# Optimization experiments

Measured on AMD Instinct MI355X. Metric: run time of the kernel, lower is better.

## Reference

```python
import jax, jax.numpy as jnp
import numpy as np

N_NODES = 100000
N_EDGES = 1600000
D_IN = 128
D_HID = 128
N_CLASSES = 4
N_GRAPHS = 512


def setup_inputs() -> dict:
    key = jax.random.key(0)
    ks = jax.random.split(key, 10)
    x = jax.random.normal(ks[0], (N_NODES, D_IN), dtype=jnp.float32)
    edge_index = jax.random.randint(ks[1], (2, N_EDGES), 0, N_NODES, dtype=jnp.int64)
    batch = jnp.sort(jax.random.randint(ks[2], (N_NODES,), 0, N_GRAPHS, dtype=jnp.int64))
    s = 1.0 / np.sqrt(D_IN)
    W1l = jax.random.uniform(ks[3], (D_HID, D_IN), jnp.float32, -s, s)
    W1r = jax.random.uniform(ks[4], (D_HID, D_IN), jnp.float32, -s, s)
    b1 = jnp.zeros((D_HID,), jnp.float32)
    s2 = 1.0 / np.sqrt(D_HID)
    W2l = jax.random.uniform(ks[5], (D_HID, D_HID), jnp.float32, -s2, s2)
    W2r = jax.random.uniform(ks[6], (D_HID, D_HID), jnp.float32, -s2, s2)
    b2 = jnp.zeros((D_HID,), jnp.float32)
    Wlin = jax.random.uniform(ks[7], (N_CLASSES, D_HID), jnp.float32, -s2, s2)
    blin = jax.random.uniform(ks[8], (N_CLASSES,), jnp.float32, -s2, s2)
    return {"x": x, "edge_index": edge_index, "batch": batch,
            "W1l": W1l, "b1": b1, "W1r": W1r,
            "W2l": W2l, "b2": b2, "W2r": W2r,
            "Wlin": Wlin, "blin": blin}


def _sage_conv(x, src, dst, deg_inv, W_l, b, W_r):
    # mean-aggregate neighbor features (messages flow src -> dst)
    agg = jax.ops.segment_sum(x[src], dst, num_segments=N_NODES) * deg_inv
    return agg @ W_l.T + b + x @ W_r.T


def reference(x, edge_index, batch, W1l, b1, W1r, W2l, b2, W2r, Wlin, blin):
    src, dst = edge_index[0], edge_index[1]
    ones = jnp.ones((src.shape[0],), x.dtype)
    deg = jax.ops.segment_sum(ones, dst, num_segments=N_NODES)
    deg_inv = (1.0 / jnp.maximum(deg, 1.0))[:, None]

    h = jax.nn.relu(_sage_conv(x, src, dst, deg_inv, W1l, b1, W1r))
    h = jax.nn.relu(_sage_conv(h, src, dst, deg_inv, W2l, b2, W2r))

    # global mean pool over graphs
    gsum = jax.ops.segment_sum(h, batch, num_segments=N_GRAPHS)
    gcnt = jax.ops.segment_sum(jnp.ones((N_NODES,), h.dtype), batch, num_segments=N_GRAPHS)
    pooled = gsum / jnp.maximum(gcnt, 1.0)[:, None]

    # dropout is identity in eval mode
    return pooled @ Wlin.T + blin
```

## Files before the change

kernel.cpp:

```cpp
#include <hip/hip_runtime.h>
#include <hip/hip_bf16.h>


#define NN 100000
#define NE 1600000
#define DH 128
#define NG 512
#define CSTRIDE 48
#define NBKT 8
#define BKT_SZ 12500
#define NSLICE 256
#define ESLICE 6250

#define PSUM_SCALE  1048576.0f
#define PSUM_INV    (1.0f/1048576.0f)

typedef __hip_bfloat16 bf16;
typedef __bf16 bf16x8 __attribute__((ext_vector_type(8)));
typedef float  f32x4  __attribute__((ext_vector_type(4)));
typedef float  f32x2  __attribute__((ext_vector_type(2)));
typedef unsigned char u8;

__device__ __forceinline__ void bf8_to_f(uint4 q, float* w) {
    union { unsigned u; float f; } t;
    t.u = q.x << 16;          w[0] = t.f;
    t.u = q.x & 0xffff0000u;  w[1] = t.f;
    t.u = q.y << 16;          w[2] = t.f;
    t.u = q.y & 0xffff0000u;  w[3] = t.f;
    t.u = q.z << 16;          w[4] = t.f;
    t.u = q.z & 0xffff0000u;  w[5] = t.f;
    t.u = q.w << 16;          w[6] = t.f;
    t.u = q.w & 0xffff0000u;  w[7] = t.f;
}

__device__ __forceinline__ unsigned pack4_fp8(float a, float b, float c, float d) {
    int p = __builtin_amdgcn_cvt_pk_fp8_f32(a, b, 0, false);
    p = __builtin_amdgcn_cvt_pk_fp8_f32(c, d, p, true);
    return (unsigned)p;
}


__global__ __launch_bounds__(256) void k_xconv(
    const float* __restrict__ x, u8* __restrict__ fq)
{
    int g = blockIdx.x * 256 + threadIdx.x;
    const float4* s = (const float4*)(x + g * 8);
    float4 u0 = s[0], u1 = s[1];
    uint2 v;
    v.x = pack4_fp8(u0.x, u0.y, u0.z, u0.w);
    v.y = pack4_fp8(u1.x, u1.y, u1.z, u1.w);
    *(uint2*)(fq + (size_t)g * 8) = v;
}

__global__ __launch_bounds__(256) void k_fill(
    const int* __restrict__ ei, int* __restrict__ deg, int* __restrict__ col)
{
    const int bucket = blockIdx.x & (NBKT - 1);
    const int wi     = blockIdx.x >> 3;
    const int lo = bucket * BKT_SZ, hi = lo + BKT_SZ;
    const int e0 = wi * ESLICE;
    for (int e = e0 + threadIdx.x; e < e0 + ESLICE; e += 256) {
        int d = __builtin_nontemporal_load(ei + NE + e);
        if (d >= lo && d < hi) {
            int s = __builtin_nontemporal_load(ei + e);
            int pos = atomicAdd(&deg[d], 1);
            if (pos < CSTRIDE) col[d * CSTRIDE + pos] = s;
        }
    }
}

__global__ __launch_bounds__(256) void k_cnt(
    const int* __restrict__ batch, int* __restrict__ cnt)
{
    int g = blockIdx.x * 256 + threadIdx.x;
    if (g >= NG) return;
    int lo0 = 0, hi0 = NN, lo1 = 0, hi1 = NN;
    while (lo0 < hi0) { int m = (lo0 + hi0) >> 1; if (batch[m] < g)     lo0 = m + 1; else hi0 = m; }
    while (lo1 < hi1) { int m = (lo1 + hi1) >> 1; if (batch[m] < g + 1) lo1 = m + 1; else hi1 = m; }
    cnt[g] = lo1 - lo0;
}

__global__ __launch_bounds__(256) void k_wconv(
    const float* __restrict__ w0, const float* __restrict__ w1,
    const float* __restrict__ w2, const float* __restrict__ w3,
    bf16* __restrict__ wb)
{
    int gid = blockIdx.x * 256 + threadIdx.x;
    int m = gid >> 14, i = gid & 16383;
    const float* src = (m == 0) ? w0 : (m == 1) ? w1 : (m == 2) ? w2 : w3;
    wb[gid] = __float2bfloat16(src[i]);
}


__global__ __launch_bounds__(256) void k_gather(
    const int* __restrict__ deg, const int* __restrict__ col,
    const u8* __restrict__ fq, bf16* __restrict__ agg)
{
    const int nid  = blockIdx.x * 4 + (threadIdx.x >> 6);
    const int lane = threadIdx.x & 63;
    const int qsub = lane >> 4;
    const int l4   = lane & 15;
    int dgr = __builtin_amdgcn_readfirstlane(deg[nid]);
    int dg = dgr > CSTRIDE ? CSTRIDE : dgr;
    int vidx = (lane < CSTRIDE) ? col[nid * CSTRIDE + lane] : 0;

    float a[8] = {0.f, 0.f, 0.f, 0.f, 0.f, 0.f, 0.f, 0.f};

    for (int e = 0; e < dg; e += 8) {
        int sa0 = __builtin_amdgcn_readlane(vidx, min(e + 0, dg - 1));
        int sa1 = __builtin_amdgcn_readlane(vidx, min(e + 1, dg - 1));
        int sa2 = __builtin_amdgcn_readlane(vidx, min(e + 2, dg - 1));
        int sa3 = __builtin_amdgcn_readlane(vidx, min(e + 3, dg - 1));
        int sb0 = __builtin_amdgcn_readlane(vidx, min(e + 4, dg - 1));
        int sb1 = __builtin_amdgcn_readlane(vidx, min(e + 5, dg - 1));
        int sb2 = __builtin_amdgcn_readlane(vidx, min(e + 6, dg - 1));
        int sb3 = __builtin_amdgcn_readlane(vidx, min(e + 7, dg - 1));
        int sA = (qsub == 0) ? sa0 : (qsub == 1) ? sa1 : (qsub == 2) ? sa2 : sa3;
        int sB = (qsub == 0) ? sb0 : (qsub == 1) ? sb1 : (qsub == 2) ? sb2 : sb3;
        float mA = (e + qsub     < dg) ? 1.f : 0.f;
        float mB = (e + 4 + qsub < dg) ? 1.f : 0.f;
        uint2 qA = *(const uint2*)(fq + (size_t)sA * DH + l4 * 8);
        uint2 qB = *(const uint2*)(fq + (size_t)sB * DH + l4 * 8);
        f32x2 v0 = __builtin_amdgcn_cvt_pk_f32_fp8((int)qA.x, false);
        f32x2 v1 = __builtin_amdgcn_cvt_pk_f32_fp8((int)qA.x, true);
        f32x2 v2 = __builtin_amdgcn_cvt_pk_f32_fp8((int)qA.y, false);
        f32x2 v3 = __builtin_amdgcn_cvt_pk_f32_fp8((int)qA.y, true);
        a[0] += v0[0] * mA; a[1] += v0[1] * mA;
        a[2] += v1[0] * mA; a[3] += v1[1] * mA;
        a[4] += v2[0] * mA; a[5] += v2[1] * mA;
        a[6] += v3[0] * mA; a[7] += v3[1] * mA;
        v0 = __builtin_amdgcn_cvt_pk_f32_fp8((int)qB.x, false);
        v1 = __builtin_amdgcn_cvt_pk_f32_fp8((int)qB.x, true);
        v2 = __builtin_amdgcn_cvt_pk_f32_fp8((int)qB.y, false);
        v3 = __builtin_amdgcn_cvt_pk_f32_fp8((int)qB.y, true);
        a[0] += v0[0] * mB; a[1] += v0[1] * mB;
        a[2] += v1[0] * mB; a[3] += v1[1] * mB;
        a[4] += v2[0] * mB; a[5] += v2[1] * mB;
        a[6] += v3[0] * mB; a[7] += v3[1] * mB;
    }

    #pragma unroll
    for (int i = 0; i < 8; ++i) {
        a[i] += __shfl_xor(a[i], 16, 64);
        a[i] += __shfl_xor(a[i], 32, 64);
    }

    if (qsub == 0) {
        float di = 1.0f / fmaxf((float)dgr, 1.0f);
        union { bf16 b[8]; uint4 u; } pk;
        #pragma unroll
        for (int i = 0; i < 8; ++i) pk.b[i] = __float2bfloat16(a[i] * di);
        *(uint4*)(agg + nid * DH + l4 * 8) = pk.u;
    }
}


#define WSTR 136

template <bool POOL>
__global__ __launch_bounds__(256, 4) void k_layer(
    const bf16* __restrict__ agg, const void* __restrict__ xop,
    const bf16* __restrict__ Wlb, const bf16* __restrict__ Wrb,
    const float* __restrict__ bias,
    u8* __restrict__ outq, int* __restrict__ psum,
    const int* __restrict__ batch)
{
    __shared__ bf16 wl[128 * WSTR];
    __shared__ int  bb[128];

    const int tid  = threadIdx.x;
    const int wave = tid >> 6;
    const int lane = tid & 63;
    const int lm   = lane & 15;
    const int kg   = lane >> 4;
    const int base = blockIdx.x * 128;
    const int wbase = base + wave * 32;

    const int r0 = min(wbase + lm,      NN - 1);
    const int r1 = min(wbase + 16 + lm, NN - 1);

    if (POOL && tid < 128) bb[tid] = batch[min(base + tid, NN - 1)];

    {
        const int row = tid >> 1, half = tid & 1;
        const uint4* src = (const uint4*)(Wlb + row * DH + half * 64);
        uint4* dst = (uint4*)(wl + row * WSTR + half * 64);
        #pragma unroll
        for (int i = 0; i < 8; ++i) dst[i] = src[i];
    }
    __syncthreads();

    f32x4 acc[2][8];
    #pragma unroll
    for (int i = 0; i < 2; ++i)
        #pragma unroll
        for (int t = 0; t < 8; ++t)
            acc[i][t] = (f32x4){0.f, 0.f, 0.f, 0.f};

    #pragma unroll
    for (int kc = 0; kc < 4; ++kc) {
        const int ko = kc * 32 + kg * 8;
        bf16x8 a0 = *(const bf16x8*)(agg + r0 * DH + ko);
        bf16x8 a1 = *(const bf16x8*)(agg + r1 * DH + ko);
        #pragma unroll
        for (int t = 0; t < 8; ++t) {
            bf16x8 b = *(const bf16x8*)(wl + (t * 16 + lm) * WSTR + ko);
            acc[0][t] = __builtin_amdgcn_mfma_f32_16x16x32_bf16(a0, b, acc[0][t], 0, 0, 0);
            acc[1][t] = __builtin_amdgcn_mfma_f32_16x16x32_bf16(a1, b, acc[1][t], 0, 0, 0);
        }
    }
    __syncthreads();

    {
        const int row = tid >> 1, half = tid & 1;
        const uint4* src = (const uint4*)(Wrb + row * DH + half * 64);
        uint4* dst = (uint4*)(wl + row * WSTR + half * 64);
        #pragma unroll
        for (int i = 0; i < 8; ++i) dst[i] = src[i];
    }
    __syncthreads();

    #pragma unroll
    for (int kc = 0; kc < 4; ++kc) {
        const int ko = kc * 32 + kg * 8;
        bf16x8 a0, a1;
        if (!POOL) {
            const float* xf = (const float*)xop;
            const float4* p0 = (const float4*)(xf + (size_t)r0 * DH + ko);
            const float4* p1 = (const float4*)(xf + (size_t)r1 * DH + ko);
            float4 u0 = p0[0], u1 = p0[1], v0 = p1[0], v1 = p1[1];
            a0[0] = (__bf16)u0.x; a0[1] = (__bf16)u0.y; a0[2] = (__bf16)u0.z; a0[3] = (__bf16)u0.w;
            a0[4] = (__bf16)u1.x; a0[5] = (__bf16)u1.y; a0[6] = (__bf16)u1.z; a0[7] = (__bf16)u1.w;
            a1[0] = (__bf16)v0.x; a1[1] = (__bf16)v0.y; a1[2] = (__bf16)v0.z; a1[3] = (__bf16)v0.w;
            a1[4] = (__bf16)v1.x; a1[5] = (__bf16)v1.y; a1[6] = (__bf16)v1.z; a1[7] = (__bf16)v1.w;
        } else {
            const u8* xq = (const u8*)xop;
            uint2 q0 = *(const uint2*)(xq + (size_t)r0 * DH + ko);
            uint2 q1 = *(const uint2*)(xq + (size_t)r1 * DH + ko);
            f32x2 c0 = __builtin_amdgcn_cvt_pk_f32_fp8((int)q0.x, false);
            f32x2 c1 = __builtin_amdgcn_cvt_pk_f32_fp8((int)q0.x, true);
            f32x2 c2 = __builtin_amdgcn_cvt_pk_f32_fp8((int)q0.y, false);
            f32x2 c3 = __builtin_amdgcn_cvt_pk_f32_fp8((int)q0.y, true);
            a0[0] = (__bf16)c0[0]; a0[1] = (__bf16)c0[1];
            a0[2] = (__bf16)c1[0]; a0[3] = (__bf16)c1[1];
            a0[4] = (__bf16)c2[0]; a0[5] = (__bf16)c2[1];
            a0[6] = (__bf16)c3[0]; a0[7] = (__bf16)c3[1];
            c0 = __builtin_amdgcn_cvt_pk_f32_fp8((int)q1.x, false);
            c1 = __builtin_amdgcn_cvt_pk_f32_fp8((int)q1.x, true);
            c2 = __builtin_amdgcn_cvt_pk_f32_fp8((int)q1.y, false);
            c3 = __builtin_amdgcn_cvt_pk_f32_fp8((int)q1.y, true);
            a1[0] = (__bf16)c0[0]; a1[1] = (__bf16)c0[1];
            a1[2] = (__bf16)c1[0]; a1[3] = (__bf16)c1[1];
            a1[4] = (__bf16)c2[0]; a1[5] = (__bf16)c2[1];
            a1[6] = (__bf16)c3[0]; a1[7] = (__bf16)c3[1];
        }
        #pragma unroll
        for (int t = 0; t < 8; ++t) {
            bf16x8 b = *(const bf16x8*)(wl + (t * 16 + lm) * WSTR + ko);
            acc[0][t] = __builtin_amdgcn_mfma_f32_16x16x32_bf16(a0, b, acc[0][t], 0, 0, 0);
            acc[1][t] = __builtin_amdgcn_mfma_f32_16x16x32_bf16(a1, b, acc[1][t], 0, 0, 0);
        }
    }
    __syncthreads();

    bf16* ob = wl;
    const int quad = lane >> 4;
    #pragma unroll
    for (int i = 0; i < 2; ++i) {
        #pragma unroll
        for (int r = 0; r < 4; ++r) {
            const int lr = wave * 32 + i * 16 + quad * 4 + r;
            const int n  = base + lr;
            #pragma unroll
            for (int t = 0; t < 8; ++t) {
                const int f = t * 16 + lm;
                float v = fmaxf(acc[i][t][r] + bias[f], 0.f);
                if (POOL && n >= NN) v = 0.f;
                ob[lr * DH + f] = __float2bfloat16(v);
            }
        }
    }
    __syncthreads();

    if (!POOL) {
        uint2* d = (uint2*)(outq + (size_t)base * DH);
        #pragma unroll
        for (int i = 0; i < 8; ++i) {
            const int idx = i * 256 + tid;
            const int n = base + (idx >> 4);
            if (n < NN) {
                uint4 s = ((const uint4*)ob)[idx];
                float w[8];
                bf8_to_f(s, w);
                uint2 o;
                o.x = pack4_fp8(w[0], w[1], w[2], w[3]);
                o.y = pack4_fp8(w[4], w[5], w[6], w[7]);
                d[idx] = o;
            }
        }
    } else {
        const int f = tid & 127, h = tid >> 7;
        float rs = 0.f;
        int cur = bb[h * 64];
        #pragma unroll 8
        for (int r = 0; r < 64; ++r) {
            const int row = h * 64 + r;
            float v = __bfloat162float(ob[row * DH + f]);
            int b = bb[row];
            if (b != cur) {
                atomicAdd(&psum[cur * DH + f], __float2int_rn(rs * PSUM_SCALE));
                rs = 0.f; cur = b;
            }
            rs += v;
        }
        atomicAdd(&psum[cur * DH + f], __float2int_rn(rs * PSUM_SCALE));
    }
}


__global__ __launch_bounds__(256) void k_final(
    const int* __restrict__ psum, const int* __restrict__ cnt,
    const float* __restrict__ Wlin, const float* __restrict__ blin,
    float* __restrict__ out)
{
    int gid = blockIdx.x * 256 + threadIdx.x;
    if (gid >= NG * 4) return;
    int gph = gid >> 2, c = gid & 3;
    const int* p = psum + gph * DH;
    const float* w = Wlin + c * DH;
    float s = 0.f;
    #pragma unroll 8
    for (int k = 0; k < DH; ++k)
        s += (float)p[k] * w[k];
    float inv = 1.0f / fmaxf((float)cnt[gph], 1.0f);
    out[gid] = s * PSUM_INV * inv + blin[c];
}

extern "C" void kernel_launch(void* const* d_in, const int* in_sizes, int n_in,
                              void* d_out, int out_size, void* d_ws, size_t ws_size,
                              hipStream_t stream) {
    const float* x     = (const float*)d_in[0];
    const int*   ei    = (const int*)d_in[1];
    const int*   batch = (const int*)d_in[2];
    const float* W1l   = (const float*)d_in[3];
    const float* b1    = (const float*)d_in[4];
    const float* W1r   = (const float*)d_in[5];
    const float* W2l   = (const float*)d_in[6];
    const float* b2    = (const float*)d_in[7];
    const float* W2r   = (const float*)d_in[8];
    const float* Wlin  = (const float*)d_in[9];
    const float* blin  = (const float*)d_in[10];
    float* out = (float*)d_out;

    char* base = (char*)d_ws;
    int*   deg  = (int*)(base + 64);
    int*   cnt  = (int*)(base + 400064);
    int*   psum = (int*)(base + 402112);
    bf16*  wb   = (bf16*)(base + 664256);
    int*   col  = (int*)(base + 795328);
    bf16*  agg  = (bf16*)(base + 19995328);
    u8*    fq   = (u8*)(base + 45595328);

    bf16* W1lb = wb;
    bf16* W1rb = wb + 16384;
    bf16* W2lb = wb + 32768;
    bf16* W2rb = wb + 49152;

    hipMemsetAsync(d_ws, 0, 664256, stream);

    k_xconv<<<NN * DH / 2048, 256, 0, stream>>>(x, fq);
    k_wconv<<<256, 256, 0, stream>>>(W1l, W1r, W2l, W2r, wb);
    k_fill<<<NSLICE * NBKT, 256, 0, stream>>>(ei, deg, col);
    k_cnt<<<2, 256, 0, stream>>>(batch, cnt);

    k_gather<<<NN / 4, 256, 0, stream>>>(deg, col, fq, agg);
    k_layer<false><<<(NN + 127) / 128, 256, 0, stream>>>(agg, x, W1lb, W1rb, b1,
                                                         fq, nullptr, nullptr);

    k_gather<<<NN / 4, 256, 0, stream>>>(deg, col, fq, agg);
    k_layer<true><<<(NN + 127) / 128, 256, 0, stream>>>(agg, fq, W2lb, W2rb, b2,
                                                        nullptr, psum, batch);

    k_final<<<8, 256, 0, stream>>>(psum, cnt, Wlin, blin, out);
}
```

Before: 356.5 us.

## Fuse prep kernels and schedule edge-fill buckets per XCC via work queue

Merges the x fp8 conversion, weight bf16 conversion and graph-count kernels into one launch to cut launch overhead. The edge-fill kernel now reads the hardware XCC id and has each block pull edge slices from a per-bucket atomic work queue, starting at its own XCC's bucket. The aim is to keep the deg and col atomics for a destination range local to one XCC's L2, reducing cross-die traffic. In exchange it adds atomic queue contention and two block-wide barriers per slice, and it relies on an XCC register read that is specific to this hardware.

```diff
diff --git a/kernel.cpp b/kernel.cpp
--- a/kernel.cpp
+++ b/kernel.cpp
@@ -40,55 +40,70 @@
 }
 
 
-__global__ __launch_bounds__(256) void k_xconv(
-    const float* __restrict__ x, u8* __restrict__ fq)
-{
-    int g = blockIdx.x * 256 + threadIdx.x;
-    const float4* s = (const float4*)(x + g * 8);
-    float4 u0 = s[0], u1 = s[1];
-    uint2 v;
-    v.x = pack4_fp8(u0.x, u0.y, u0.z, u0.w);
-    v.y = pack4_fp8(u1.x, u1.y, u1.z, u1.w);
-    *(uint2*)(fq + (size_t)g * 8) = v;
-}
-
-__global__ __launch_bounds__(256) void k_fill(
-    const int* __restrict__ ei, int* __restrict__ deg, int* __restrict__ col)
-{
-    const int bucket = blockIdx.x & (NBKT - 1);
-    const int wi     = blockIdx.x >> 3;
-    const int lo = bucket * BKT_SZ, hi = lo + BKT_SZ;
-    const int e0 = wi * ESLICE;
-    for (int e = e0 + threadIdx.x; e < e0 + ESLICE; e += 256) {
-        int d = __builtin_nontemporal_load(ei + NE + e);
-        if (d >= lo && d < hi) {
-            int s = __builtin_nontemporal_load(ei + e);
-            int pos = atomicAdd(&deg[d], 1);
-            if (pos < CSTRIDE) col[d * CSTRIDE + pos] = s;
-        }
-    }
-}
-
-__global__ __launch_bounds__(256) void k_cnt(
-    const int* __restrict__ batch, int* __restrict__ cnt)
-{
-    int g = blockIdx.x * 256 + threadIdx.x;
-    if (g >= NG) return;
-    int lo0 = 0, hi0 = NN, lo1 = 0, hi1 = NN;
-    while (lo0 < hi0) { int m = (lo0 + hi0) >> 1; if (batch[m] < g)     lo0 = m + 1; else hi0 = m; }
-    while (lo1 < hi1) { int m = (lo1 + hi1) >> 1; if (batch[m] < g + 1) lo1 = m + 1; else hi1 = m; }
-    cnt[g] = lo1 - lo0;
-}
-
-__global__ __launch_bounds__(256) void k_wconv(
+__global__ __launch_bounds__(256) void k_prep2(
+    const float* __restrict__ x, u8* __restrict__ fq,
     const float* __restrict__ w0, const float* __restrict__ w1,
     const float* __restrict__ w2, const float* __restrict__ w3,
-    bf16* __restrict__ wb)
-{
-    int gid = blockIdx.x * 256 + threadIdx.x;
-    int m = gid >> 14, i = gid & 16383;
-    const float* src = (m == 0) ? w0 : (m == 1) ? w1 : (m == 2) ? w2 : w3;
-    wb[gid] = __float2bfloat16(src[i]);
+    bf16* __restrict__ wb,
+    const int* __restrict__ batch, int* __restrict__ cnt)
+{
+    const int bid = blockIdx.x, tid = threadIdx.x;
+
+    {
+        int g = bid * 256 + tid;
+        const float4* s = (const float4*)(x + (size_t)g * 8);
+        float4 u0 = s[0], u1 = s[1];
+        uint2 v;
+        v.x = pack4_fp8(u0.x, u0.y, u0.z, u0.w);
+        v.y = pack4_fp8(u1.x, u1.y, u1.z, u1.w);
+        *(uint2*)(fq + (size_t)g * 8) = v;
+    }
+
+    if (bid < 256) {
+        int gid = bid * 256 + tid;
+        int m = gid >> 14, i = gid & 16383;
+        const float* src = (m == 0) ? w0 : (m == 1) ? w1 : (m == 2) ? w2 : w3;
+        wb[gid] = __float2bfloat16(src[i]);
+    } else if (bid < 258) {
+        int g = (bid - 256) * 256 + tid;
+        if (g < NG) {
+            int lo0 = 0, hi0 = NN, lo1 = 0, hi1 = NN;
+            while (lo0 < hi0) { int m = (lo0 + hi0) >> 1; if (batch[m] < g)     lo0 = m + 1; else hi0 = m; }
+            while (lo1 < hi1) { int m = (lo1 + hi1) >> 1; if (batch[m] < g + 1) lo1 = m + 1; else hi1 = m; }
+            cnt[g] = lo1 - lo0;
+        }
+    }
+}
+
+__global__ __launch_bounds__(256) void k_fill(
+    const int* __restrict__ ei, int* __restrict__ deg, int* __restrict__ col,
+    int* __restrict__ q)
+{
+    __shared__ int sl;
+    unsigned xcc;
+    asm volatile("s_getreg_b32 %0, hwreg(HW_REG_XCC_ID)" : "=s"(xcc));
+    xcc &= (NBKT - 1);
+
+    for (int a = 0; a < NBKT; ++a) {
+        const int b = (xcc + a) & (NBKT - 1);
+        const int lo = b * BKT_SZ, hi = lo + BKT_SZ;
+        for (;;) {
+            if (threadIdx.x == 0) sl = atomicAdd(&q[b], 1);
+            __syncthreads();
+            const int s0 = sl;
+            __syncthreads();
+            if (s0 >= NSLICE) break;
+            const int e0 = s0 * ESLICE;
+            for (int e = e0 + threadIdx.x; e < e0 + ESLICE; e += 256) {
+                int d = __builtin_nontemporal_load(ei + NE + e);
+                if (d >= lo && d < hi) {
+                    int s = __builtin_nontemporal_load(ei + e);
+                    int pos = atomicAdd(&deg[d], 1);
+                    if (pos < CSTRIDE) col[d * CSTRIDE + pos] = s;
+                }
+            }
+        }
+    }
 }
 
 
@@ -353,6 +368,7 @@
     float* out = (float*)d_out;
 
     char* base = (char*)d_ws;
+    int*   q    = (int*)(base);
     int*   deg  = (int*)(base + 64);
     int*   cnt  = (int*)(base + 400064);
     int*   psum = (int*)(base + 402112);
@@ -368,10 +384,8 @@
 
     hipMemsetAsync(d_ws, 0, 664256, stream);
 
-    k_xconv<<<NN * DH / 2048, 256, 0, stream>>>(x, fq);
-    k_wconv<<<256, 256, 0, stream>>>(W1l, W1r, W2l, W2r, wb);
-    k_fill<<<NSLICE * NBKT, 256, 0, stream>>>(ei, deg, col);
-    k_cnt<<<2, 256, 0, stream>>>(batch, cnt);
+    k_prep2<<<6250, 256, 0, stream>>>(x, fq, W1l, W1r, W2l, W2r, wb, batch, cnt);
+    k_fill<<<2048, 256, 0, stream>>>(ei, deg, col, q);
 
     k_gather<<<NN / 4, 256, 0, stream>>>(deg, col, fq, agg);
     k_layer<false><<<(NN + 127) / 128, 256, 0, stream>>>(agg, x, W1lb, W1rb, b1,
```

New measurement: 544.3 us. +52.7%, slower.
